# Performance work log

Measured on AMD Instinct MI355X. Metric: run time of the kernel, lower is better.

Reference implementation:

```python
import jax, jax.numpy as jnp
from jax import lax
import numpy as np
import math

NUM_CLASSES = 81
N_PER_IMG = 1024
NUM_IMAGES = 8
SCORE_THRESH = 0.05
NMS_THRESH = 0.5
DETS_PER_IMG = 100
WX, WY, WW, WH = 10.0, 10.0, 5.0, 5.0
BBOX_XFORM_CLIP = math.log(1000.0 / 16.0)


def setup_inputs() -> dict:
    key = jax.random.key(0)
    k1, k2, k3, k4 = jax.random.split(key, 4)
    M = NUM_IMAGES * N_PER_IMG
    H, W = 800, 1333
    class_logits = jax.random.normal(k1, (M, NUM_CLASSES), dtype=jnp.float32) * 3.0
    box_regression = jax.random.normal(k2, (M, 4 * NUM_CLASSES), dtype=jnp.float32) * 0.5
    # valid xyxy proposals inside the image
    xy1 = jax.random.uniform(k3, (M, 2), dtype=jnp.float32) * jnp.array([W * 0.7, H * 0.7], jnp.float32)
    wh = jax.random.uniform(k4, (M, 2), dtype=jnp.float32) * jnp.array([W * 0.3, H * 0.3], jnp.float32) + 4.0
    proposals = jnp.concatenate([xy1, xy1 + wh], axis=1)
    return {"class_logits": class_logits, "box_regression": box_regression,
            "proposals": proposals, "height": H, "width": W}


def _decode(rel_codes, boxes):
    widths = boxes[:, 2] - boxes[:, 0] + 1.0
    heights = boxes[:, 3] - boxes[:, 1] + 1.0
    ctr_x = boxes[:, 0] + 0.5 * widths
    ctr_y = boxes[:, 1] + 0.5 * heights
    rel = rel_codes.reshape(rel_codes.shape[0], -1, 4)  # [M, C, 4]
    dx = rel[:, :, 0] / WX
    dy = rel[:, :, 1] / WY
    dw = jnp.minimum(rel[:, :, 2] / WW, BBOX_XFORM_CLIP)
    dh = jnp.minimum(rel[:, :, 3] / WH, BBOX_XFORM_CLIP)
    pctr_x = dx * widths[:, None] + ctr_x[:, None]
    pctr_y = dy * heights[:, None] + ctr_y[:, None]
    pw = jnp.exp(dw) * widths[:, None]
    ph = jnp.exp(dh) * heights[:, None]
    return jnp.stack([pctr_x - 0.5 * pw, pctr_y - 0.5 * ph,
                      pctr_x + 0.5 * pw - 1.0, pctr_y + 0.5 * ph - 1.0], axis=-1)


def _clip(boxes, height, width):
    # boxes [..., 4] xyxy, clamp to [0, W-1] x [0, H-1]
    x = jnp.clip(boxes[..., 0::2], 0.0, float(width - 1))
    y = jnp.clip(boxes[..., 1::2], 0.0, float(height - 1))
    return jnp.stack([x[..., 0], y[..., 0], x[..., 1], y[..., 1]], axis=-1)


def _iou_matrix(b):
    x1, y1, x2, y2 = b[:, 0], b[:, 1], b[:, 2], b[:, 3]
    area = (x2 - x1 + 1.0) * (y2 - y1 + 1.0)
    xx1 = jnp.maximum(x1[:, None], x1[None, :])
    yy1 = jnp.maximum(y1[:, None], y1[None, :])
    xx2 = jnp.minimum(x2[:, None], x2[None, :])
    yy2 = jnp.minimum(y2[:, None], y2[None, :])
    inter = jnp.clip(xx2 - xx1 + 1.0, 0.0) * jnp.clip(yy2 - yy1 + 1.0, 0.0)
    return inter / (area[:, None] + area[None, :] - inter)


def _per_class(scores_j, boxes_j):
    # scores_j [N], boxes_j [N,4] -> sorted scores/boxes + greedy-NMS keep mask
    N = scores_j.shape[0]
    valid = scores_j > SCORE_THRESH
    s = jnp.where(valid, scores_j, 0.0)  # softmax scores are > 0
    order = jnp.argsort(-s)
    s_sorted = s[order]
    b_sorted = boxes_j[order]
    valid_sorted = valid[order]
    iou = _iou_matrix(b_sorted)  # [N, N]
    idxs = jnp.arange(N)

    def body(i, keep):
        sup = (iou[i] > NMS_THRESH) & keep[i] & (idxs > i)
        return keep & ~sup

    keep = lax.fori_loop(0, N, body, valid_sorted)
    return s_sorted, b_sorted, keep


def _per_image(prob_i, boxes_i):
    # prob_i [N, C], boxes_i [N, C, 4]; skip background class 0
    C = prob_i.shape[1]
    fg_scores = prob_i[:, 1:].T                      # [C-1, N]
    fg_boxes = jnp.swapaxes(boxes_i[:, 1:, :], 0, 1)  # [C-1, N, 4]
    s_sorted, b_sorted, keep = jax.vmap(_per_class)(fg_scores, fg_boxes)
    labels = jnp.broadcast_to(jnp.arange(1, C, dtype=jnp.int32)[:, None], s_sorted.shape)
    flat_s = jnp.where(keep, s_sorted, 0.0).reshape(-1)
    vals, idx = lax.top_k(flat_s, DETS_PER_IMG)      # detections-per-image limit
    boxes_out = b_sorted.reshape(-1, 4)[idx]
    labels_out = labels.reshape(-1)[idx]
    ok = vals > SCORE_THRESH
    return (jnp.where(ok, vals, 0.0),
            jnp.where(ok[:, None], boxes_out, 0.0),
            jnp.where(ok, labels_out, 0))


def reference(class_logits, box_regression, proposals, height, width):
    prob = jax.nn.softmax(class_logits, axis=-1)          # [M, C]
    dec = _decode(box_regression, proposals)              # [M, C, 4]
    dec = _clip(dec, height, width)
    B, N, C = NUM_IMAGES, N_PER_IMG, NUM_CLASSES
    prob = prob.reshape(B, N, C)
    dec = dec.reshape(B, N, C, 4)
    scores, boxes, labels = lax.map(lambda a: _per_image(a[0], a[1]), (prob, dec))
    return scores, boxes, labels
```

## Files before the change

kernel.cpp:

```cpp
#include <hip/hip_runtime.h>
#include <stdint.h>
#include <math.h>

#define NCLS 81
#define NFG  80
#define NPI  1024
#define NIMG 8
#define DETS 100
#define SCORE_T 0.05f
#define NMS_T   0.5f
#define NCAND   (NFG * DETS)
#define CAND_CAP 2048
#define FASTN 256

static constexpr float BBOX_CLIP = 4.1351665567423557f;

__global__ __launch_bounds__(256) void softmax_stats(
    const float* __restrict__ logits, float* __restrict__ rowmax,
    float* __restrict__ den, int M)
{
    int m = blockIdx.x * blockDim.x + threadIdx.x;
    if (m >= M) return;
    const float* r = logits + (size_t)m * NCLS;
    float mx = r[0];
    #pragma unroll
    for (int j = 1; j < NCLS; ++j) mx = fmaxf(mx, r[j]);
    float s = 0.f;
    #pragma unroll
    for (int j = 0; j < NCLS; ++j) s += expf(r[j] - mx);
    rowmax[m] = mx;
    den[m] = s;
}

__global__ __launch_bounds__(256) void per_class_nms(
    const float* __restrict__ logits, const float* __restrict__ boxreg,
    const float* __restrict__ props, const float* __restrict__ rowmax,
    const float* __restrict__ den, const int* __restrict__ hptr,
    const int* __restrict__ wptr, int* __restrict__ out_cnt,
    float* __restrict__ out_score, unsigned* __restrict__ out_key,
    float* __restrict__ out_box)
{
    int pid = blockIdx.x;
    int img = pid / NFG;
    int c   = pid % NFG;
    int cls = c + 1;

    __shared__ float box_lds[NPI][4];
    __shared__ unsigned long long key[NPI];
    __shared__ int keep[NPI];
    __shared__ float sbox[FASTN][4];
    __shared__ float sarea[FASTN];
    __shared__ unsigned long long mask[FASTN][FASTN/64];
    __shared__ unsigned long long keepw[FASTN/64];
    __shared__ unsigned wpre[4];
    __shared__ int cnt;

    float W1 = (float)(*wptr - 1);
    float H1 = (float)(*hptr - 1);

    if (threadIdx.x == 0) cnt = 0;
    for (int i = threadIdx.x; i < NPI; i += blockDim.x) key[i] = 0ULL;
    __syncthreads();

    for (int m = threadIdx.x; m < NPI; m += blockDim.x) {
        int g = img * NPI + m;
        float prob = expf(logits[(size_t)g * NCLS + cls] - rowmax[g]) / den[g];
        if (prob > SCORE_T) {
            float x1 = props[g * 4 + 0], y1 = props[g * 4 + 1];
            float x2 = props[g * 4 + 2], y2 = props[g * 4 + 3];
            float w  = x2 - x1 + 1.0f, h = y2 - y1 + 1.0f;
            float cx = x1 + 0.5f * w,  cy = y1 + 0.5f * h;
            const float* rc = boxreg + (size_t)g * (4 * NCLS) + 4 * cls;
            float dx = rc[0] / 10.0f, dy = rc[1] / 10.0f;
            float dw = fminf(rc[2] / 5.0f, BBOX_CLIP);
            float dh = fminf(rc[3] / 5.0f, BBOX_CLIP);
            float pcx = dx * w + cx, pcy = dy * h + cy;
            float pw = expf(dw) * w, ph = expf(dh) * h;
            float bx1 = pcx - 0.5f * pw;
            float by1 = pcy - 0.5f * ph;
            float bx2 = pcx + 0.5f * pw - 1.0f;
            float by2 = pcy + 0.5f * ph - 1.0f;
            bx1 = fminf(fmaxf(bx1, 0.f), W1);
            bx2 = fminf(fmaxf(bx2, 0.f), W1);
            by1 = fminf(fmaxf(by1, 0.f), H1);
            by2 = fminf(fmaxf(by2, 0.f), H1);
            box_lds[m][0] = bx1; box_lds[m][1] = by1;
            box_lds[m][2] = bx2; box_lds[m][3] = by2;
            int p = atomicAdd(&cnt, 1);
            unsigned fb = __float_as_uint(prob);
            key[p] = ((unsigned long long)fb << 32) | (unsigned)(NPI - 1 - m);
        }
    }
    __syncthreads();
    int n = cnt;

    int P = 2;
    while (P < n) P <<= 1;
    if (n > 1) {
        for (int k = 2; k <= P; k <<= 1) {
            for (int j = k >> 1; j > 0; j >>= 1) {
                for (int i = threadIdx.x; i < P; i += blockDim.x) {
                    int ixj = i ^ j;
                    if (ixj > i) {
                        unsigned long long a = key[i], b = key[ixj];
                        bool up = (i & k) == 0;
                        if (up ? (a < b) : (a > b)) { key[i] = b; key[ixj] = a; }
                    }
                }
                __syncthreads();
            }
        }
    }

    for (int i = threadIdx.x; i < NPI; i += blockDim.x) keep[i] = 0;
    __syncthreads();

    if (n <= FASTN) {
        for (int i = threadIdx.x; i < n; i += blockDim.x) {
            int mi = NPI - 1 - (int)(key[i] & 0xFFFFFFFFu);
            float bx1 = box_lds[mi][0], by1 = box_lds[mi][1];
            float bx2 = box_lds[mi][2], by2 = box_lds[mi][3];
            sbox[i][0] = bx1; sbox[i][1] = by1; sbox[i][2] = bx2; sbox[i][3] = by2;
            sarea[i] = (bx2 - bx1 + 1.f) * (by2 - by1 + 1.f);
        }
        __syncthreads();
        int nwords = ((n + 63) >> 6);
        for (int w = threadIdx.x; w < n * (FASTN/64); w += blockDim.x) {
            int i = w >> 2, wb = w & 3;
            if (wb >= nwords || ((wb + 1) << 6) - 1 <= i) { mask[i][wb] = 0ULL; continue; }
            float ax1 = sbox[i][0], ay1 = sbox[i][1];
            float ax2 = sbox[i][2], ay2 = sbox[i][3];
            float aarea = sarea[i];
            unsigned long long bits = 0ULL;
            int jbase = wb << 6;
            #pragma unroll 4
            for (int b = 0; b < 64; ++b) {
                int j = jbase + b;
                if (j < n && j > i) {
                    float bx1 = sbox[j][0], by1 = sbox[j][1];
                    float bx2 = sbox[j][2], by2 = sbox[j][3];
                    float xx1 = fmaxf(ax1, bx1), yy1 = fmaxf(ay1, by1);
                    float xx2 = fminf(ax2, bx2), yy2 = fminf(ay2, by2);
                    float iw = fmaxf(xx2 - xx1 + 1.f, 0.f);
                    float ih = fmaxf(yy2 - yy1 + 1.f, 0.f);
                    float inter = iw * ih;
                    float iou = inter / (aarea + sarea[j] - inter);
                    if (iou > NMS_T) bits |= (1ULL << b);
                }
            }
            mask[i][wb] = bits;
        }
        __syncthreads();
        if (threadIdx.x < 64) {
            int lane = threadIdx.x;
            unsigned long long kb = 0ULL;
            if (lane < 4) {
                int rem = n - (lane << 6);
                if (rem >= 64) kb = ~0ULL;
                else if (rem > 0) kb = (1ULL << rem) - 1ULL;
            }
            unsigned long long rm = 0ULL;
            for (int i = 0; i < n; ++i) {
                unsigned long long rw = __shfl(rm, i >> 6, 64);
                if (!((rw >> (i & 63)) & 1ULL)) {
                    unsigned long long mrow = (lane < 4) ? mask[i][lane] : 0ULL;
                    rm |= mrow;
                }
            }
            if (lane < 4) keepw[lane] = kb & ~rm;
        }
        __syncthreads();
        for (int i = threadIdx.x; i < n; i += blockDim.x)
            keep[i] = (int)((keepw[i >> 6] >> (i & 63)) & 1ULL);
        __syncthreads();
    } else {
        for (int i = threadIdx.x; i < n; i += blockDim.x) keep[i] = 1;
        __syncthreads();
        for (int i = 0; i < n; ++i) {
            if (keep[i]) {
                unsigned long long ki = key[i];
                int mi = NPI - 1 - (int)(ki & 0xFFFFFFFFu);
                float ax1 = box_lds[mi][0], ay1 = box_lds[mi][1];
                float ax2 = box_lds[mi][2], ay2 = box_lds[mi][3];
                float aarea = (ax2 - ax1 + 1.f) * (ay2 - ay1 + 1.f);
                for (int jj = i + 1 + (int)threadIdx.x; jj < n; jj += blockDim.x) {
                    if (keep[jj]) {
                        int mj = NPI - 1 - (int)(key[jj] & 0xFFFFFFFFu);
                        float bx1 = box_lds[mj][0], by1 = box_lds[mj][1];
                        float bx2 = box_lds[mj][2], by2 = box_lds[mj][3];
                        float xx1 = fmaxf(ax1, bx1), yy1 = fmaxf(ay1, by1);
                        float xx2 = fminf(ax2, bx2), yy2 = fminf(ay2, by2);
                        float iw = fmaxf(xx2 - xx1 + 1.f, 0.f);
                        float ih = fmaxf(yy2 - yy1 + 1.f, 0.f);
                        float inter = iw * ih;
                        float barea = (bx2 - bx1 + 1.f) * (by2 - by1 + 1.f);
                        float iou = inter / (aarea + barea - inter);
                        if (iou > NMS_T) keep[jj] = 0;
                    }
                }
            }
            __syncthreads();
        }
    }

    {
        int t = threadIdx.x, lane = t & 63, w = t >> 6;
        int k0 = keep[4 * t], k1 = keep[4 * t + 1];
        int k2 = keep[4 * t + 2], k3 = keep[4 * t + 3];
        unsigned s = (unsigned)(k0 + k1 + k2 + k3);
        unsigned v = s;
        #pragma unroll
        for (int off = 1; off < 64; off <<= 1) {
            unsigned u = __shfl_up(v, off, 64);
            v += (lane >= off) ? u : 0u;
        }
        if (lane == 63) wpre[w] = v;
        __syncthreads();
        unsigned woff = 0;
        for (int w2 = 0; w2 < w; ++w2) woff += wpre[w2];
        unsigned before = v + woff - s;
        unsigned r = before;
        #pragma unroll
        for (int j = 0; j < 4; ++j) {
            int i = 4 * t + j;
            int kv = (j == 0) ? k0 : (j == 1) ? k1 : (j == 2) ? k2 : k3;
            if (kv && r < DETS) {
                unsigned long long ki = key[i];
                int mi = NPI - 1 - (int)(ki & 0xFFFFFFFFu);
                int slot = pid * DETS + (int)r;
                out_score[slot] = __uint_as_float((unsigned)(ki >> 32));
                out_key[slot] = (unsigned)(c * NPI + i);
                out_box[slot * 4 + 0] = box_lds[mi][0];
                out_box[slot * 4 + 1] = box_lds[mi][1];
                out_box[slot * 4 + 2] = box_lds[mi][2];
                out_box[slot * 4 + 3] = box_lds[mi][3];
            }
            r += (unsigned)kv;
        }
        if (t == 0) {
        }
        __syncthreads();
        if (t == 0) {
            unsigned tot = wpre[0] + wpre[1] + wpre[2] + wpre[3];
            out_cnt[pid] = (int)(tot < DETS ? tot : DETS);
        }
    }
}

__device__ __forceinline__ void suffix_select(
    unsigned* hist, unsigned* wtot, int K, int* outB, unsigned* outAbove)
{
    int t = threadIdx.x, lane = t & 63, w = t >> 6;
    unsigned c0 = hist[4 * t], c1 = hist[4 * t + 1];
    unsigned c2 = hist[4 * t + 2], c3 = hist[4 * t + 3];
    unsigned ps = c0 + c1 + c2 + c3;
    unsigned v = ps;
    #pragma unroll
    for (int off = 1; off < 64; off <<= 1) {
        unsigned u = __shfl_down(v, off, 64);
        v += (lane + off < 64) ? u : 0u;
    }
    if (lane == 0) wtot[w] = v;
    __syncthreads();
    unsigned woff = 0;
    for (int w2 = w + 1; w2 < 16; ++w2) woff += wtot[w2];
    unsigned Sown = v + woff;
    unsigned A3 = Sown - ps;
    unsigned A2 = A3 + c3, A1 = A2 + c2, A0 = A1 + c1;
    unsigned A[4] = {A0, A1, A2, A3};
    unsigned C[4] = {c0, c1, c2, c3};
    #pragma unroll
    for (int j = 0; j < 4; ++j) {
        if ((int)A[j] < K && (int)(A[j] + C[j]) >= K) {
            *outB = 4 * t + j;
            *outAbove = A[j];
        }
    }
    __syncthreads();
}

__global__ __launch_bounds__(1024) void topk_merge(
    const int* __restrict__ cnts, const float* __restrict__ escore,
    const unsigned* __restrict__ ekey, const float* __restrict__ ebox,
    float* __restrict__ out)
{
    int img = blockIdx.x;
    __shared__ unsigned sc[NCAND];
    __shared__ unsigned hist[4096];
    __shared__ unsigned long long cand[CAND_CAP];
    __shared__ unsigned wtot[16];
    __shared__ int sB1, sB2, sNc;
    __shared__ unsigned sAb1, sAb2;

    int t = threadIdx.x;
    if (t == 0) { sB1 = 0; sB2 = 0; sNc = 0; sAb1 = 0; sAb2 = 0; }
    for (int p = t; p < NCAND; p += 1024) {
        int cc = p / DETS, k = p % DETS;
        unsigned fb = 0;
        if (k < cnts[img * NFG + cc]) fb = __float_as_uint(escore[img * NCAND + p]);
        sc[p] = fb;
    }
    for (int i = t; i < 4096; i += 1024) hist[i] = 0;
    __syncthreads();

    for (int p = t; p < NCAND; p += 1024) {
        unsigned fb = sc[p];
        if (fb) atomicAdd(&hist[fb >> 19], 1u);
    }
    __syncthreads();
    suffix_select(hist, wtot, DETS, &sB1, &sAb1);
    int B1 = sB1;
    unsigned ab1 = sAb1;

    for (int i = t; i < 4096; i += 1024) hist[i] = 0;
    __syncthreads();
    for (int p = t; p < NCAND; p += 1024) {
        unsigned fb = sc[p];
        if (fb && (int)(fb >> 19) == B1) atomicAdd(&hist[(fb >> 7) & 0xFFFu], 1u);
    }
    __syncthreads();
    suffix_select(hist, wtot, DETS - (int)ab1, &sB2, &sAb2);
    int B2 = sB2;

    for (int p = t; p < NCAND; p += 1024) {
        unsigned fb = sc[p];
        if (fb) {
            int d1 = (int)(fb >> 19);
            bool ok = d1 > B1 || (d1 == B1 && (int)((fb >> 7) & 0xFFFu) >= B2);
            if (ok) {
                int pos = atomicAdd(&sNc, 1);
                if (pos < CAND_CAP) {
                    unsigned fk = ekey[img * NCAND + p];
                    unsigned low = ((0x1FFFFu - fk) << 13) | (unsigned)p;
                    cand[pos] = ((unsigned long long)fb << 32) | low;
                }
            }
        }
    }
    __syncthreads();
    int nc = sNc < CAND_CAP ? sNc : CAND_CAP;
    int P = 128;
    while (P < nc) P <<= 1;
    for (int i = t; i < P; i += 1024)
        if (i >= nc) cand[i] = 0ULL;
    __syncthreads();

    for (int k = 2; k <= P; k <<= 1) {
        for (int j = k >> 1; j > 0; j >>= 1) {
            for (int i = t; i < P; i += 1024) {
                int ixj = i ^ j;
                if (ixj > i) {
                    unsigned long long a = cand[i], b = cand[ixj];
                    bool up = (i & k) == 0;
                    if (up ? (a < b) : (a > b)) { cand[i] = b; cand[ixj] = a; }
                }
            }
            __syncthreads();
        }
    }

    float* oScore = out;
    float* oBox   = out + NIMG * DETS;
    float* oLab   = out + NIMG * DETS * 5;

    if (t < DETS) {
        unsigned long long b = cand[t];
        int o = img * DETS + t;
        if (b != 0ULL) {
            float scv = __uint_as_float((unsigned)(b >> 32));
            unsigned low = (unsigned)(b & 0xFFFFFFFFu);
            unsigned flatkey = 0x1FFFFu - ((low >> 13) & 0x1FFFFu);
            int p = (int)(low & 0x1FFFu);
            int gp = img * NCAND + p;
            oScore[o] = scv;
            oBox[o * 4 + 0] = ebox[gp * 4 + 0];
            oBox[o * 4 + 1] = ebox[gp * 4 + 1];
            oBox[o * 4 + 2] = ebox[gp * 4 + 2];
            oBox[o * 4 + 3] = ebox[gp * 4 + 3];
            oLab[o] = (float)((flatkey >> 10) + 1);
        } else {
            oScore[o] = 0.f;
            oBox[o * 4 + 0] = 0.f; oBox[o * 4 + 1] = 0.f;
            oBox[o * 4 + 2] = 0.f; oBox[o * 4 + 3] = 0.f;
            oLab[o] = 0.f;
        }
    }
}

extern "C" void kernel_launch(void* const* d_in, const int* in_sizes, int n_in,
                              void* d_out, int out_size, void* d_ws, size_t ws_size,
                              hipStream_t stream) {
    const float* logits = (const float*)d_in[0];
    const float* boxreg = (const float*)d_in[1];
    const float* props  = (const float*)d_in[2];
    const int*   hptr   = (const int*)d_in[3];
    const int*   wptr   = (const int*)d_in[4];
    float* out = (float*)d_out;
    int M = in_sizes[0] / NCLS;

    char* ws = (char*)d_ws;
    float*    rowmax = (float*)ws;    ws += (size_t)M * sizeof(float);
    float*    den    = (float*)ws;    ws += (size_t)M * sizeof(float);
    int*      cnt    = (int*)ws;      ws += (size_t)NIMG * NFG * sizeof(int);
    float*    escore = (float*)ws;    ws += (size_t)NIMG * NCAND * sizeof(float);
    unsigned* ekey   = (unsigned*)ws; ws += (size_t)NIMG * NCAND * sizeof(unsigned);
    float*    ebox   = (float*)ws;    ws += (size_t)NIMG * NCAND * 4 * sizeof(float);

    softmax_stats<<<(M + 255) / 256, 256, 0, stream>>>(logits, rowmax, den, M);
    per_class_nms<<<NIMG * NFG, 256, 0, stream>>>(
        logits, boxreg, props, rowmax, den, hptr, wptr, cnt, escore, ekey, ebox);
    topk_merge<<<NIMG, 1024, 0, stream>>>(cnt, escore, ekey, ebox, out);
}
```

Measured before the change: 61.42 us.

## Precompute transposed class probabilities and add single-wavefront NMS path for small counts

The softmax kernel now stages logits in shared memory and writes a class-major probability matrix, so the per-class NMS blocks read probabilities with coalesced float4 loads instead of strided logits reads plus recomputed exp. Proposals and box deltas are also fetched as float4. When a class has at most 64 candidates, a single wavefront sorts with shuffle-based bitonic sort and runs greedy NMS through ballots, skipping the shared-memory sort, mask build and the many block barriers. This costs an extra workspace buffer of 80*M floats that is written and then read back.

```diff
diff --git a/kernel.cpp b/kernel.cpp
--- a/kernel.cpp
+++ b/kernel.cpp
@@ -12,33 +12,48 @@
 #define NCAND   (NFG * DETS)
 #define CAND_CAP 2048
 #define FASTN 256
+#define ROWS 64
 
 static constexpr float BBOX_CLIP = 4.1351665567423557f;
 
-__global__ __launch_bounds__(256) void softmax_stats(
-    const float* __restrict__ logits, float* __restrict__ rowmax,
-    float* __restrict__ den, int M)
+__global__ __launch_bounds__(256) void softmax_probT(
+    const float* __restrict__ logits, float* __restrict__ probT, int M)
 {
-    int m = blockIdx.x * blockDim.x + threadIdx.x;
-    if (m >= M) return;
-    const float* r = logits + (size_t)m * NCLS;
-    float mx = r[0];
-    #pragma unroll
-    for (int j = 1; j < NCLS; ++j) mx = fmaxf(mx, r[j]);
-    float s = 0.f;
-    #pragma unroll
-    for (int j = 0; j < NCLS; ++j) s += expf(r[j] - mx);
-    rowmax[m] = mx;
-    den[m] = s;
+    __shared__ float tile[ROWS * NCLS];
+    __shared__ float mx[ROWS], dn[ROWS];
+    int t = threadIdx.x;
+    int rbase = blockIdx.x * ROWS;
+
+    for (int idx = t; idx < ROWS * NCLS; idx += 256)
+        tile[idx] = logits[(size_t)rbase * NCLS + idx];
+    __syncthreads();
+
+    if (t < ROWS) {
+        const float* r = tile + t * NCLS;
+        float m = r[0];
+        #pragma unroll
+        for (int j = 1; j < NCLS; ++j) m = fmaxf(m, r[j]);
+        float s = 0.f;
+        #pragma unroll
+        for (int j = 0; j < NCLS; ++j) s += expf(r[j] - m);
+        mx[t] = m; dn[t] = s;
+    }
+    __syncthreads();
+
+    for (int o = t; o < ROWS * NFG; o += 256) {
+        int r = o & 63;
+        int c = o >> 6;
+        float v = expf(tile[r * NCLS + (c + 1)] - mx[r]) / dn[r];
+        probT[(size_t)c * M + rbase + r] = v;
+    }
 }
 
 __global__ __launch_bounds__(256) void per_class_nms(
-    const float* __restrict__ logits, const float* __restrict__ boxreg,
-    const float* __restrict__ props, const float* __restrict__ rowmax,
-    const float* __restrict__ den, const int* __restrict__ hptr,
+    const float* __restrict__ probT, const float* __restrict__ boxreg,
+    const float* __restrict__ props, const int* __restrict__ hptr,
     const int* __restrict__ wptr, int* __restrict__ out_cnt,
     float* __restrict__ out_score, unsigned* __restrict__ out_key,
-    float* __restrict__ out_box)
+    float* __restrict__ out_box, int M)
 {
     int pid = blockIdx.x;
     int img = pid / NFG;
@@ -55,68 +70,133 @@
     __shared__ unsigned wpre[4];
     __shared__ int cnt;
 
+    int t = threadIdx.x;
     float W1 = (float)(*wptr - 1);
     float H1 = (float)(*hptr - 1);
 
-    if (threadIdx.x == 0) cnt = 0;
-    for (int i = threadIdx.x; i < NPI; i += blockDim.x) key[i] = 0ULL;
-    __syncthreads();
-
-    for (int m = threadIdx.x; m < NPI; m += blockDim.x) {
-        int g = img * NPI + m;
-        float prob = expf(logits[(size_t)g * NCLS + cls] - rowmax[g]) / den[g];
-        if (prob > SCORE_T) {
-            float x1 = props[g * 4 + 0], y1 = props[g * 4 + 1];
-            float x2 = props[g * 4 + 2], y2 = props[g * 4 + 3];
-            float w  = x2 - x1 + 1.0f, h = y2 - y1 + 1.0f;
-            float cx = x1 + 0.5f * w,  cy = y1 + 0.5f * h;
-            const float* rc = boxreg + (size_t)g * (4 * NCLS) + 4 * cls;
-            float dx = rc[0] / 10.0f, dy = rc[1] / 10.0f;
-            float dw = fminf(rc[2] / 5.0f, BBOX_CLIP);
-            float dh = fminf(rc[3] / 5.0f, BBOX_CLIP);
-            float pcx = dx * w + cx, pcy = dy * h + cy;
-            float pw = expf(dw) * w, ph = expf(dh) * h;
-            float bx1 = pcx - 0.5f * pw;
-            float by1 = pcy - 0.5f * ph;
-            float bx2 = pcx + 0.5f * pw - 1.0f;
-            float by2 = pcy + 0.5f * ph - 1.0f;
-            bx1 = fminf(fmaxf(bx1, 0.f), W1);
-            bx2 = fminf(fmaxf(bx2, 0.f), W1);
-            by1 = fminf(fmaxf(by1, 0.f), H1);
-            by2 = fminf(fmaxf(by2, 0.f), H1);
-            box_lds[m][0] = bx1; box_lds[m][1] = by1;
-            box_lds[m][2] = bx2; box_lds[m][3] = by2;
-            int p = atomicAdd(&cnt, 1);
-            unsigned fb = __float_as_uint(prob);
-            key[p] = ((unsigned long long)fb << 32) | (unsigned)(NPI - 1 - m);
+    if (t == 0) cnt = 0;
+    for (int i = t; i < NPI; i += 256) key[i] = 0ULL;
+    __syncthreads();
+
+    {
+        const float4 pv = *(const float4*)(probT + (size_t)c * M + img * NPI + 4 * t);
+        float pr[4] = {pv.x, pv.y, pv.z, pv.w};
+        #pragma unroll
+        for (int j = 0; j < 4; ++j) {
+            if (pr[j] > SCORE_T) {
+                int m = 4 * t + j;
+                int g = img * NPI + m;
+                const float4 pb = *(const float4*)(props + (size_t)g * 4);
+                float x1 = pb.x, y1 = pb.y, x2 = pb.z, y2 = pb.w;
+                float w  = x2 - x1 + 1.0f, h = y2 - y1 + 1.0f;
+                float cx = x1 + 0.5f * w,  cy = y1 + 0.5f * h;
+                const float4 rc = *(const float4*)(boxreg + (size_t)g * (4 * NCLS) + 4 * cls);
+                float dx = rc.x / 10.0f, dy = rc.y / 10.0f;
+                float dw = fminf(rc.z / 5.0f, BBOX_CLIP);
+                float dh = fminf(rc.w / 5.0f, BBOX_CLIP);
+                float pcx = dx * w + cx, pcy = dy * h + cy;
+                float pw = expf(dw) * w, ph = expf(dh) * h;
+                float bx1 = pcx - 0.5f * pw;
+                float by1 = pcy - 0.5f * ph;
+                float bx2 = pcx + 0.5f * pw - 1.0f;
+                float by2 = pcy + 0.5f * ph - 1.0f;
+                bx1 = fminf(fmaxf(bx1, 0.f), W1);
+                bx2 = fminf(fmaxf(bx2, 0.f), W1);
+                by1 = fminf(fmaxf(by1, 0.f), H1);
+                by2 = fminf(fmaxf(by2, 0.f), H1);
+                box_lds[m][0] = bx1; box_lds[m][1] = by1;
+                box_lds[m][2] = bx2; box_lds[m][3] = by2;
+                int p = atomicAdd(&cnt, 1);
+                unsigned fb = __float_as_uint(pr[j]);
+                key[p] = ((unsigned long long)fb << 32) | (unsigned)(NPI - 1 - m);
+            }
         }
     }
     __syncthreads();
     int n = cnt;
+
+    if (n <= 64) {
+        if (t < 64) {
+            int lane = t;
+            unsigned long long k = (lane < n) ? key[lane] : 0ULL;
+            #pragma unroll
+            for (int kk = 2; kk <= 64; kk <<= 1) {
+                #pragma unroll
+                for (int j = kk >> 1; j > 0; j >>= 1) {
+                    unsigned long long o = __shfl_xor(k, j, 64);
+                    bool up = ((lane & kk) == 0);
+                    bool lower = ((lane & j) == 0);
+                    bool take_max = (up == lower);
+                    k = take_max ? (k > o ? k : o) : (k < o ? k : o);
+                }
+            }
+            bool valid = (lane < n);
+            float bx1 = 0.f, by1 = 0.f, bx2 = 0.f, by2 = 0.f, area = 0.f;
+            if (valid) {
+                int mi = NPI - 1 - (int)(k & 0xFFFFFFFFu);
+                bx1 = box_lds[mi][0]; by1 = box_lds[mi][1];
+                bx2 = box_lds[mi][2]; by2 = box_lds[mi][3];
+                area = (bx2 - bx1 + 1.f) * (by2 - by1 + 1.f);
+            }
+            unsigned long long sup = 0ULL;
+            for (int i = 0; i < n; ++i) {
+                bool alive = !((sup >> i) & 1ULL);
+                float ax1 = __shfl(bx1, i, 64), ay1 = __shfl(by1, i, 64);
+                float ax2 = __shfl(bx2, i, 64), ay2 = __shfl(by2, i, 64);
+                float aarea = __shfl(area, i, 64);
+                bool s = false;
+                if (alive && valid && lane > i) {
+                    float xx1 = fmaxf(ax1, bx1), yy1 = fmaxf(ay1, by1);
+                    float xx2 = fminf(ax2, bx2), yy2 = fminf(ay2, by2);
+                    float iw = fmaxf(xx2 - xx1 + 1.f, 0.f);
+                    float ih = fmaxf(yy2 - yy1 + 1.f, 0.f);
+                    float inter = iw * ih;
+                    float iou = inter / (aarea + area - inter);
+                    s = iou > NMS_T;
+                }
+                sup |= __ballot(s);
+            }
+            bool kept = valid && !((sup >> lane) & 1ULL);
+            unsigned long long keptm = __ballot(kept);
+            int rank = __popcll(keptm & ((1ULL << lane) - 1ULL));
+            if (kept && rank < DETS) {
+                int slot = pid * DETS + rank;
+                out_score[slot] = __uint_as_float((unsigned)(k >> 32));
+                out_key[slot] = (unsigned)(c * NPI + lane);
+                out_box[slot * 4 + 0] = bx1;
+                out_box[slot * 4 + 1] = by1;
+                out_box[slot * 4 + 2] = bx2;
+                out_box[slot * 4 + 3] = by2;
+            }
+            if (lane == 0) {
+                int tot = __popcll(keptm);
+                out_cnt[pid] = tot < DETS ? tot : DETS;
+            }
+        }
+        return;
+    }
 
     int P = 2;
     while (P < n) P <<= 1;
-    if (n > 1) {
-        for (int k = 2; k <= P; k <<= 1) {
-            for (int j = k >> 1; j > 0; j >>= 1) {
-                for (int i = threadIdx.x; i < P; i += blockDim.x) {
-                    int ixj = i ^ j;
-                    if (ixj > i) {
-                        unsigned long long a = key[i], b = key[ixj];
-                        bool up = (i & k) == 0;
-                        if (up ? (a < b) : (a > b)) { key[i] = b; key[ixj] = a; }
-                    }
-                }
-                __syncthreads();
-            }
-        }
-    }
-
-    for (int i = threadIdx.x; i < NPI; i += blockDim.x) keep[i] = 0;
+    for (int k = 2; k <= P; k <<= 1) {
+        for (int j = k >> 1; j > 0; j >>= 1) {
+            for (int i = t; i < P; i += 256) {
+                int ixj = i ^ j;
+                if (ixj > i) {
+                    unsigned long long a = key[i], b = key[ixj];
+                    bool up = (i & k) == 0;
+                    if (up ? (a < b) : (a > b)) { key[i] = b; key[ixj] = a; }
+                }
+            }
+            __syncthreads();
+        }
+    }
+
+    for (int i = t; i < NPI; i += 256) keep[i] = 0;
     __syncthreads();
 
     if (n <= FASTN) {
-        for (int i = threadIdx.x; i < n; i += blockDim.x) {
+        for (int i = t; i < n; i += 256) {
             int mi = NPI - 1 - (int)(key[i] & 0xFFFFFFFFu);
             float bx1 = box_lds[mi][0], by1 = box_lds[mi][1];
             float bx2 = box_lds[mi][2], by2 = box_lds[mi][3];
@@ -125,7 +205,7 @@
         }
         __syncthreads();
         int nwords = ((n + 63) >> 6);
-        for (int w = threadIdx.x; w < n * (FASTN/64); w += blockDim.x) {
+        for (int w = t; w < n * (FASTN/64); w += 256) {
             int i = w >> 2, wb = w & 3;
             if (wb >= nwords || ((wb + 1) << 6) - 1 <= i) { mask[i][wb] = 0ULL; continue; }
             float ax1 = sbox[i][0], ay1 = sbox[i][1];
@@ -151,8 +231,8 @@
             mask[i][wb] = bits;
         }
         __syncthreads();
-        if (threadIdx.x < 64) {
-            int lane = threadIdx.x;
+        if (t < 64) {
+            int lane = t;
             unsigned long long kb = 0ULL;
             if (lane < 4) {
                 int rem = n - (lane << 6);
@@ -170,11 +250,11 @@
             if (lane < 4) keepw[lane] = kb & ~rm;
         }
         __syncthreads();
-        for (int i = threadIdx.x; i < n; i += blockDim.x)
+        for (int i = t; i < n; i += 256)
             keep[i] = (int)((keepw[i >> 6] >> (i & 63)) & 1ULL);
         __syncthreads();
     } else {
-        for (int i = threadIdx.x; i < n; i += blockDim.x) keep[i] = 1;
+        for (int i = t; i < n; i += 256) keep[i] = 1;
         __syncthreads();
         for (int i = 0; i < n; ++i) {
             if (keep[i]) {
@@ -183,7 +263,7 @@
                 float ax1 = box_lds[mi][0], ay1 = box_lds[mi][1];
                 float ax2 = box_lds[mi][2], ay2 = box_lds[mi][3];
                 float aarea = (ax2 - ax1 + 1.f) * (ay2 - ay1 + 1.f);
-                for (int jj = i + 1 + (int)threadIdx.x; jj < n; jj += blockDim.x) {
+                for (int jj = i + 1 + t; jj < n; jj += 256) {
                     if (keep[jj]) {
                         int mj = NPI - 1 - (int)(key[jj] & 0xFFFFFFFFu);
                         float bx1 = box_lds[mj][0], by1 = box_lds[mj][1];
@@ -204,7 +284,7 @@
     }
 
     {
-        int t = threadIdx.x, lane = t & 63, w = t >> 6;
+        int lane = t & 63, w = t >> 6;
         int k0 = keep[4 * t], k1 = keep[4 * t + 1];
         int k2 = keep[4 * t + 2], k3 = keep[4 * t + 3];
         unsigned s = (unsigned)(k0 + k1 + k2 + k3);
@@ -236,8 +316,6 @@
                 out_box[slot * 4 + 3] = box_lds[mi][3];
             }
             r += (unsigned)kv;
-        }
-        if (t == 0) {
         }
         __syncthreads();
         if (t == 0) {
@@ -399,15 +477,14 @@
     int M = in_sizes[0] / NCLS;
 
     char* ws = (char*)d_ws;
-    float*    rowmax = (float*)ws;    ws += (size_t)M * sizeof(float);
-    float*    den    = (float*)ws;    ws += (size_t)M * sizeof(float);
+    float*    probT  = (float*)ws;    ws += (size_t)NFG * M * sizeof(float);
     int*      cnt    = (int*)ws;      ws += (size_t)NIMG * NFG * sizeof(int);
     float*    escore = (float*)ws;    ws += (size_t)NIMG * NCAND * sizeof(float);
     unsigned* ekey   = (unsigned*)ws; ws += (size_t)NIMG * NCAND * sizeof(unsigned);
     float*    ebox   = (float*)ws;    ws += (size_t)NIMG * NCAND * 4 * sizeof(float);
 
-    softmax_stats<<<(M + 255) / 256, 256, 0, stream>>>(logits, rowmax, den, M);
+    softmax_probT<<<M / ROWS, 256, 0, stream>>>(logits, probT, M);
     per_class_nms<<<NIMG * NFG, 256, 0, stream>>>(
-        logits, boxreg, props, rowmax, den, hptr, wptr, cnt, escore, ekey, ebox);
+        probT, boxreg, props, hptr, wptr, cnt, escore, ekey, ebox, M);
     topk_merge<<<NIMG, 1024, 0, stream>>>(cnt, escore, ekey, ebox, out);
 }
```

New measurement: 61.07 us (median of 2 runs). About the same (-0.6%).
